# Kernel tuning notes

Measured on AMD Instinct MI355X. Metric: run time of the kernel, lower is better.

## Reference

```python
import jax, jax.numpy as jnp
import numpy as np


def setup_inputs() -> dict:
    key = jax.random.key(0)
    ks = jax.random.split(key, 5)
    B, D, L, NH = 2, 1024, 2048, 8
    H = D // NH  # number of SSM heads / filter channels
    return {
        "v": jax.random.normal(ks[0], (B, D, L), jnp.float32),
        "k": jax.random.normal(ks[1], (H, L), jnp.float32) * 0.1,
        "bias": jax.random.normal(ks[2], (D,), jnp.float32),
        "x1": jax.random.normal(ks[3], (B, D, L), jnp.float32),
        "x2": jax.random.normal(ks[4], (B, D, L), jnp.float32),
        "num_heads": NH,
    }


def reference(v, k, bias, x1, x2, num_heads):
    # Multi-head Hyena FFT long conv with fused gating (safari fftconv_h3 semantics):
    #   kv[b,h,d1,d2,l] = v[b,h,d1,l] * x2[b,h,d2,l]
    #   y = causal_fftconv(kv, k[h]) + bias[h,d1] * kv
    #   out[b,h,d2,l] = sum_d1 y[b,h,d1,d2,l] * x1[b,h,d1,l]
    B, D, L = v.shape
    H = D // num_heads
    fft_size = 2 * L  # zero-pad to 2L for linear (causal) convolution
    vr = v.reshape(B, H, num_heads, L)
    x1r = x1.reshape(B, H, num_heads, L)
    x2r = x2.reshape(B, H, num_heads, L)
    kv = vr[:, :, :, None, :] * x2r[:, :, None, :, :]  # (B, H, d1, d2, L)
    k_f = jnp.fft.rfft(k.astype(jnp.float32), n=fft_size)  # (H, fft_size//2+1)
    y = jnp.fft.irfft(
        jnp.fft.rfft(kv, n=fft_size) * k_f[None, :, None, None, :], n=fft_size
    )[..., :L]  # (B, H, d1, d2, L)
    skip = bias.astype(jnp.float32).reshape(H, num_heads)[None, :, :, None, None]
    y = y + kv * skip
    out = jnp.einsum("bhijl,bhil->bhjl", y, x1r)  # contract d1 with q-gate
    return out.reshape(B, D, L)
```

## Files before the change

### kernel.cpp

```cpp
#include <hip/hip_runtime.h>
#include <stdint.h>


typedef __attribute__((ext_vector_type(8))) short bf16x8;
typedef __attribute__((ext_vector_type(4))) float f32x4;

#define NHd  8
#define SC   128
#define PLS  40
#define GW   192

static __device__ __forceinline__ uint32_t pkbf(float a, float b) {
    const uint32_t ua = __float_as_uint(a) + 0x8000u;
    const uint32_t ub = __float_as_uint(b) + 0x8000u;
    return __builtin_amdgcn_perm(ub, ua, 0x07060302u);
}

union U8 { uint32_t u[4]; bf16x8 v; uint4 q; };

__global__ __launch_bounds__(256, 5) void hyena_mfma5_kernel(
    const float* __restrict__ v, const float* __restrict__ kf,
    const float* __restrict__ bias, const float* __restrict__ x1,
    const float* __restrict__ x2, float* __restrict__ out,
    int B, int H, int L)
{
    __shared__ __align__(16) float  ks[2048];
    __shared__ __align__(16) float4 gwin[GW];
    __shared__ __align__(16) ushort vT[2][SC][NHd];
    __shared__ __align__(16) ushort x2T[2][NHd][136];
    __shared__ __align__(16) ushort Pl[4][2][16][PLS];
    __shared__ float sbuf[2][64];

    const int tid  = threadIdx.x;
    const int h    = blockIdx.x;
    const int l0b  = ((int)gridDim.y - 1 - (int)blockIdx.y) * 64;
    const int nk   = l0b + 64;

    const int lane = tid & 63, wv = tid >> 6;
    const int lq   = lane & 15, quad = lane >> 4;
    const int wb   = wv >> 1;
    const int wl0  = l0b + (wv & 1) * 32;
    const int baseb = (wb * H + h) * NHd * L;

    for (int i = tid; i < nk; i += 256) ks[i] = kf[h * L + i];

    bf16x8 xf0 = {}, xf1 = {};
    if (quad == 0) {
        float a0[NHd], a1[NHd];
#pragma unroll
        for (int d1 = 0; d1 < NHd; ++d1) {
            a0[d1] = x1[baseb + d1 * L + wl0 + lq];
            a1[d1] = x1[baseb + d1 * L + wl0 + 16 + lq];
        }
        U8 u0, u1;
#pragma unroll
        for (int j = 0; j < 4; ++j) {
            u0.u[j] = pkbf(a0[2 * j], a0[2 * j + 1]);
            u1.u[j] = pkbf(a1[2 * j], a1[2 * j + 1]);
        }
        xf0 = u0.v; xf1 = u1.v;
    }

    if (tid < 128) {
        const int bb = tid >> 6, l = tid & 63;
        const int bs = (bb * H + h) * NHd * L;
        float s = 0.f;
#pragma unroll
        for (int d1 = 0; d1 < NHd; ++d1)
            s += bias[h * NHd + d1] * x1[bs + d1 * L + l0b + l]
                                    * v [bs + d1 * L + l0b + l];
        sbuf[bb][l] = s;
    }

    f32x4 acc0 = {0.f, 0.f, 0.f, 0.f}, acc1 = {0.f, 0.f, 0.f, 0.f};
    const int wlmax = wl0 + 31;
    const int ebase = 127 + (wv & 1) * 32 + lq - 4 * quad;

    for (int s0 = 0; s0 < nk; s0 += SC) {
        __syncthreads();
        {
            const int bb = tid >> 7, row = tid & 127;
            const int bs = (bb * H + h) * NHd * L;
            const float* vp = v + bs + s0 + row;
            float f[NHd];
#pragma unroll
            for (int d1 = 0; d1 < NHd; ++d1) f[d1] = vp[d1 * L];
            *(uint4*)&vT[bb][row][0] = make_uint4(
                pkbf(f[0], f[1]), pkbf(f[2], f[3]),
                pkbf(f[4], f[5]), pkbf(f[6], f[7]));

            const int d2 = row >> 4, ms = (row & 15) * 8;
            const float* xp = x2 + bs + d2 * L + s0 + ms;
            const float4 q0 = *(const float4*)xp;
            const float4 q1 = *(const float4*)(xp + 4);
            *(uint4*)&x2T[bb][d2][ms] = make_uint4(
                pkbf(q0.x, q0.y), pkbf(q0.z, q0.w),
                pkbf(q1.x, q1.y), pkbf(q1.z, q1.w));
        }
        if (tid < GW - 1) {
            const int i = l0b - s0 - 127 + tid;
            float4 w = {0.f, 0.f, 0.f, 0.f};
            if (i >= 3) {
                w.x = ks[i]; w.y = ks[i - 1]; w.z = ks[i - 2]; w.w = ks[i - 3];
            } else if (i >= 0) {
                w.x = ks[i];
                if (i >= 1) w.y = ks[i - 1];
                if (i >= 2) w.z = ks[i - 2];
            }
            gwin[tid] = w;
        }
        __syncthreads();

        const int cmax = min(SC, wlmax - s0 + 1);
        for (int c = 0; c < cmax; c += 32) {
            bf16x8 av0 = {}, av1 = {};
            if (quad == 0) {
                av0 = *(const bf16x8*)&vT[wb][c + lq][0];
                av1 = *(const bf16x8*)&vT[wb][c + 16 + lq][0];
            }
            const int ge = ebase - c;
            const float4 g00 = *(const float4*)&gwin[ge];
            const float4 g01 = *(const float4*)&gwin[ge - 16];
            const float4 g10 = *(const float4*)&gwin[ge + 16];
            const bf16x8 bx = *(const bf16x8*)&x2T[wb][lq & 7][c + 8 * quad];

            const f32x4 Z = {0.f, 0.f, 0.f, 0.f};
            const f32x4 S00 = __builtin_amdgcn_mfma_f32_16x16x32_bf16(av0, xf0, Z, 0, 0, 0);
            const f32x4 S01 = __builtin_amdgcn_mfma_f32_16x16x32_bf16(av1, xf0, Z, 0, 0, 0);
            const f32x4 S10 = __builtin_amdgcn_mfma_f32_16x16x32_bf16(av0, xf1, Z, 0, 0, 0);
            const f32x4 S11 = __builtin_amdgcn_mfma_f32_16x16x32_bf16(av1, xf1, Z, 0, 0, 0);

            uint2 w;
            w.x = pkbf(S00[0] * g00.x, S00[1] * g00.y);
            w.y = pkbf(S00[2] * g00.z, S00[3] * g00.w);
            *(uint2*)&Pl[wv][0][lq][4 * quad] = w;
            w.x = pkbf(S01[0] * g01.x, S01[1] * g01.y);
            w.y = pkbf(S01[2] * g01.z, S01[3] * g01.w);
            *(uint2*)&Pl[wv][0][lq][16 + 4 * quad] = w;
            w.x = pkbf(S10[0] * g10.x, S10[1] * g10.y);
            w.y = pkbf(S10[2] * g10.z, S10[3] * g10.w);
            *(uint2*)&Pl[wv][1][lq][4 * quad] = w;
            w.x = pkbf(S11[0] * g00.x, S11[1] * g00.y);
            w.y = pkbf(S11[2] * g00.z, S11[3] * g00.w);
            *(uint2*)&Pl[wv][1][lq][16 + 4 * quad] = w;

            const bf16x8 ap0 = *(const bf16x8*)&Pl[wv][0][lq][8 * quad];
            acc0 = __builtin_amdgcn_mfma_f32_16x16x32_bf16(ap0, bx, acc0, 0, 0, 0);
            const bf16x8 ap1 = *(const bf16x8*)&Pl[wv][1][lq][8 * quad];
            acc1 = __builtin_amdgcn_mfma_f32_16x16x32_bf16(ap1, bx, acc1, 0, 0, 0);
        }
    }

    if (lq < NHd) {
        const int lloc = (wv & 1) * 32 + quad * 4;
        const float* xr = x2 + baseb + lq * L + wl0 + quad * 4;
        float* orow = out + baseb + lq * L + wl0 + quad * 4;
        float4 o0, o1;
        o0.x = acc0[0] + xr[0] * sbuf[wb][lloc + 0];
        o0.y = acc0[1] + xr[1] * sbuf[wb][lloc + 1];
        o0.z = acc0[2] + xr[2] * sbuf[wb][lloc + 2];
        o0.w = acc0[3] + xr[3] * sbuf[wb][lloc + 3];
        o1.x = acc1[0] + xr[16] * sbuf[wb][lloc + 16];
        o1.y = acc1[1] + xr[17] * sbuf[wb][lloc + 17];
        o1.z = acc1[2] + xr[18] * sbuf[wb][lloc + 18];
        o1.w = acc1[3] + xr[19] * sbuf[wb][lloc + 19];
        *(float4*)orow = o0;
        *(float4*)(orow + 16) = o1;
    }
}

extern "C" void kernel_launch(void* const* d_in, const int* in_sizes, int n_in,
                              void* d_out, int out_size, void* d_ws, size_t ws_size,
                              hipStream_t stream) {
    const float* v    = (const float*)d_in[0];
    const float* k    = (const float*)d_in[1];
    const float* bias = (const float*)d_in[2];
    const float* x1   = (const float*)d_in[3];
    const float* x2   = (const float*)d_in[4];
    float* out = (float*)d_out;

    const int D = in_sizes[2];
    const int H = D / NHd;
    const int L = in_sizes[1] / H;
    const int B = in_sizes[0] / (D * L);

    dim3 grid(H, L / 64);
    hyena_mfma5_kernel<<<grid, 256, 0, stream>>>(v, k, bias, x1, x2, out, B, H, L);
}
```

Before: 177.6 us.

## Keep gated scores in registers by swapping MFMA operand roles and permuting x2 layout

The second MFMA now takes x2 as the A operand and the gated score fragments as the B operand. The score tiles no longer round-trip through the Pl shared-memory scratch, so that buffer and its LDS stores and loads are removed. To match the new operand layout, x2 is written to LDS in a permuted column order, and the epilogue writes the transposed accumulator layout with scalar stores. It also reuses one gate window load across iterations and raises the launch-bounds occupancy hint from 5 to 6. In exchange the output stores become scalar and uncoalesced-looking, and the tighter register budget may cause spills.

Result: faster. 158.8 us (-10.6%).

```diff
diff --git a/kernel.cpp b/kernel.cpp
--- a/kernel.cpp
+++ b/kernel.cpp
@@ -7,7 +7,6 @@
 
 #define NHd  8
 #define SC   128
-#define PLS  40
 #define GW   192
 
 static __device__ __forceinline__ uint32_t pkbf(float a, float b) {
@@ -18,7 +17,7 @@
 
 union U8 { uint32_t u[4]; bf16x8 v; uint4 q; };
 
-__global__ __launch_bounds__(256, 5) void hyena_mfma5_kernel(
+__global__ __launch_bounds__(256, 6) void hyena_mfma6_kernel(
     const float* __restrict__ v, const float* __restrict__ kf,
     const float* __restrict__ bias, const float* __restrict__ x1,
     const float* __restrict__ x2, float* __restrict__ out,
@@ -28,7 +27,6 @@
     __shared__ __align__(16) float4 gwin[GW];
     __shared__ __align__(16) ushort vT[2][SC][NHd];
     __shared__ __align__(16) ushort x2T[2][NHd][136];
-    __shared__ __align__(16) ushort Pl[4][2][16][PLS];
     __shared__ float sbuf[2][64];
 
     const int tid  = threadIdx.x;
@@ -76,6 +74,9 @@
     const int wlmax = wl0 + 31;
     const int ebase = 127 + (wv & 1) * 32 + lq - 4 * quad;
 
+    bool gfirst = true;
+    float4 g10c = {0.f, 0.f, 0.f, 0.f};
+
     for (int s0 = 0; s0 < nk; s0 += SC) {
         __syncthreads();
         {
@@ -90,12 +91,16 @@
                 pkbf(f[4], f[5]), pkbf(f[6], f[7]));
 
             const int d2 = row >> 4, ms = (row & 15) * 8;
+            const int G = ms & ~31;
+            const int o = ms & 31;
+            const int pa = ((o >> 2) & 3) * 8 + (o >> 4) * 4;
             const float* xp = x2 + bs + d2 * L + s0 + ms;
             const float4 q0 = *(const float4*)xp;
             const float4 q1 = *(const float4*)(xp + 4);
-            *(uint4*)&x2T[bb][d2][ms] = make_uint4(
-                pkbf(q0.x, q0.y), pkbf(q0.z, q0.w),
-                pkbf(q1.x, q1.y), pkbf(q1.z, q1.w));
+            *(uint2*)&x2T[bb][d2][G + pa] =
+                make_uint2(pkbf(q0.x, q0.y), pkbf(q0.z, q0.w));
+            *(uint2*)&x2T[bb][d2][G + pa + 8] =
+                make_uint2(pkbf(q1.x, q1.y), pkbf(q1.z, q1.w));
         }
         if (tid < GW - 1) {
             const int i = l0b - s0 - 127 + tid;
@@ -119,10 +124,13 @@
                 av1 = *(const bf16x8*)&vT[wb][c + 16 + lq][0];
             }
             const int ge = ebase - c;
+            float4 g10;
+            if (gfirst) { g10 = *(const float4*)&gwin[ge + 16]; gfirst = false; }
+            else        g10 = g10c;
             const float4 g00 = *(const float4*)&gwin[ge];
             const float4 g01 = *(const float4*)&gwin[ge - 16];
-            const float4 g10 = *(const float4*)&gwin[ge + 16];
-            const bf16x8 bx = *(const bf16x8*)&x2T[wb][lq & 7][c + 8 * quad];
+            g10c = g01;
+            const bf16x8 ax = *(const bf16x8*)&x2T[wb][lq & 7][c + 8 * quad];
 
             const f32x4 Z = {0.f, 0.f, 0.f, 0.f};
             const f32x4 S00 = __builtin_amdgcn_mfma_f32_16x16x32_bf16(av0, xf0, Z, 0, 0, 0);
@@ -130,42 +138,32 @@
             const f32x4 S10 = __builtin_amdgcn_mfma_f32_16x16x32_bf16(av0, xf1, Z, 0, 0, 0);
             const f32x4 S11 = __builtin_amdgcn_mfma_f32_16x16x32_bf16(av1, xf1, Z, 0, 0, 0);
 
-            uint2 w;
-            w.x = pkbf(S00[0] * g00.x, S00[1] * g00.y);
-            w.y = pkbf(S00[2] * g00.z, S00[3] * g00.w);
-            *(uint2*)&Pl[wv][0][lq][4 * quad] = w;
-            w.x = pkbf(S01[0] * g01.x, S01[1] * g01.y);
-            w.y = pkbf(S01[2] * g01.z, S01[3] * g01.w);
-            *(uint2*)&Pl[wv][0][lq][16 + 4 * quad] = w;
-            w.x = pkbf(S10[0] * g10.x, S10[1] * g10.y);
-            w.y = pkbf(S10[2] * g10.z, S10[3] * g10.w);
-            *(uint2*)&Pl[wv][1][lq][4 * quad] = w;
-            w.x = pkbf(S11[0] * g00.x, S11[1] * g00.y);
-            w.y = pkbf(S11[2] * g00.z, S11[3] * g00.w);
-            *(uint2*)&Pl[wv][1][lq][16 + 4 * quad] = w;
+            U8 p0, p1;
+            p0.u[0] = pkbf(S00[0] * g00.x, S00[1] * g00.y);
+            p0.u[1] = pkbf(S00[2] * g00.z, S00[3] * g00.w);
+            p0.u[2] = pkbf(S01[0] * g01.x, S01[1] * g01.y);
+            p0.u[3] = pkbf(S01[2] * g01.z, S01[3] * g01.w);
+            p1.u[0] = pkbf(S10[0] * g10.x, S10[1] * g10.y);
+            p1.u[1] = pkbf(S10[2] * g10.z, S10[3] * g10.w);
+            p1.u[2] = pkbf(S11[0] * g00.x, S11[1] * g00.y);
+            p1.u[3] = pkbf(S11[2] * g00.z, S11[3] * g00.w);
 
-            const bf16x8 ap0 = *(const bf16x8*)&Pl[wv][0][lq][8 * quad];
-            acc0 = __builtin_amdgcn_mfma_f32_16x16x32_bf16(ap0, bx, acc0, 0, 0, 0);
-            const bf16x8 ap1 = *(const bf16x8*)&Pl[wv][1][lq][8 * quad];
-            acc1 = __builtin_amdgcn_mfma_f32_16x16x32_bf16(ap1, bx, acc1, 0, 0, 0);
+            acc0 = __builtin_amdgcn_mfma_f32_16x16x32_bf16(ax, p0.v, acc0, 0, 0, 0);
+            acc1 = __builtin_amdgcn_mfma_f32_16x16x32_bf16(ax, p1.v, acc1, 0, 0, 0);
         }
     }
 
-    if (lq < NHd) {
-        const int lloc = (wv & 1) * 32 + quad * 4;
-        const float* xr = x2 + baseb + lq * L + wl0 + quad * 4;
-        float* orow = out + baseb + lq * L + wl0 + quad * 4;
-        float4 o0, o1;
-        o0.x = acc0[0] + xr[0] * sbuf[wb][lloc + 0];
-        o0.y = acc0[1] + xr[1] * sbuf[wb][lloc + 1];
-        o0.z = acc0[2] + xr[2] * sbuf[wb][lloc + 2];
-        o0.w = acc0[3] + xr[3] * sbuf[wb][lloc + 3];
-        o1.x = acc1[0] + xr[16] * sbuf[wb][lloc + 16];
-        o1.y = acc1[1] + xr[17] * sbuf[wb][lloc + 17];
-        o1.z = acc1[2] + xr[18] * sbuf[wb][lloc + 18];
-        o1.w = acc1[3] + xr[19] * sbuf[wb][lloc + 19];
-        *(float4*)orow = o0;
-        *(float4*)(orow + 16) = o1;
+    if (quad < 2) {
+        const int d2b = 4 * quad;
+        const int lA  = wl0 + lq;
+        const float sb0 = sbuf[wb][(wv & 1) * 32 + lq];
+        const float sb1 = sbuf[wb][(wv & 1) * 32 + 16 + lq];
+#pragma unroll
+        for (int r = 0; r < 4; ++r) {
+            const int ro = baseb + (d2b + r) * L + lA;
+            out[ro]      = acc0[r] + x2[ro]      * sb0;
+            out[ro + 16] = acc1[r] + x2[ro + 16] * sb1;
+        }
     }
 }
 
@@ -185,5 +183,5 @@
     const int B = in_sizes[0] / (D * L);
 
     dim3 grid(H, L / 64);
-    hyena_mfma5_kernel<<<grid, 256, 0, stream>>>(v, k, bias, x1, x2, out, B, H, L);
+    hyena_mfma6_kernel<<<grid, 256, 0, stream>>>(v, k, bias, x1, x2, out, B, H, L);
 }
```
